# Kernel optimization log

Measured on AMD Instinct MI355X. Metric: run time of the kernel, lower is better.

The kernel has to match this reference:

```python
import jax, jax.numpy as jnp
import numpy as np

N = 100000
E = 1600000
DIN = 64
DH = 64
C = 16


def _sage_conv(x, edge_index, W_l, W_r, b):
    # PyG SAGEConv (aggr='mean'): out = lin_l(mean_{j in N(i)} x_j) + lin_r(x_i)
    src, dst = edge_index[0], edge_index[1]
    msgs = x[src]                                   # [E, D] gather
    num_nodes = x.shape[0]
    agg = jax.ops.segment_sum(msgs, dst, num_segments=num_nodes)      # [N, D]
    deg = jax.ops.segment_sum(jnp.ones((msgs.shape[0],), x.dtype), dst,
                              num_segments=num_nodes)                 # [N]
    mean = agg / jnp.maximum(deg, 1.0)[:, None]
    return mean @ W_l + b + x @ W_r


def setup_inputs() -> dict:
    key = jax.random.key(0)
    ks = jax.random.split(key, 8)
    x = jax.random.normal(ks[0], (N, DIN), dtype=jnp.float32)
    edge_index = jax.random.randint(ks[1], (2, E), 0, N, dtype=jnp.int64)
    s = 1.0 / np.sqrt(DIN)
    W1_l = jax.random.normal(ks[2], (DIN, DH), dtype=jnp.float32) * s
    W1_r = jax.random.normal(ks[3], (DIN, DH), dtype=jnp.float32) * s
    b1 = jnp.zeros((DH,), jnp.float32)
    sh = 1.0 / np.sqrt(DH)
    W2_l = jax.random.normal(ks[4], (DH, C), dtype=jnp.float32) * sh
    W2_r = jax.random.normal(ks[5], (DH, C), dtype=jnp.float32) * sh
    b2 = jnp.zeros((C,), jnp.float32)
    return {"x": x, "edge_index": edge_index, "W1_l": W1_l, "W1_r": W1_r,
            "b1": b1, "W2_l": W2_l, "W2_r": W2_r, "b2": b2}


def reference(x, edge_index, W1_l, W1_r, b1, W2_l, W2_r, b2):
    h = _sage_conv(x, edge_index, W1_l, W1_r, b1)
    h = jax.nn.relu(h)
    # dropout is identity at inference
    out = _sage_conv(h, edge_index, W2_l, W2_r, b2)
    return out
```

## Files before the change

### kernel.cpp

```cpp
#include <hip/hip_runtime.h>
#include <hip/hip_fp16.h>

#define NB 256
#define CHUNK 8192

__global__ void k_cvt(const float* __restrict__ x, __half* __restrict__ xh, int total) {
  int i = (blockIdx.x * 256 + threadIdx.x) * 8;
  if (i >= total) return;
  float4 a = *(const float4*)(x + i);
  float4 b = *(const float4*)(x + i + 4);
  __half2* dst = (__half2*)(xh + i);
  dst[0] = __floats2half2_rn(a.x, a.y);
  dst[1] = __floats2half2_rn(a.z, a.w);
  dst[2] = __floats2half2_rn(b.x, b.y);
  dst[3] = __floats2half2_rn(b.z, b.w);
}

__global__ void k_part(const int* __restrict__ srcI, const int* __restrict__ dstI,
                       int* __restrict__ gcur, int* __restrict__ pairs,
                       int E, int N, int capN, int capE) {
  __shared__ int hist[NB];
  __shared__ int base[NB];
  __shared__ int cnt[NB];
  int tid = threadIdx.x;
  int e0 = blockIdx.x * CHUNK;
  int eend = min(e0 + CHUNK, E);
  hist[tid] = 0;
  __syncthreads();
  for (int e = e0 + tid; e < eend; e += 256) {
    int d = dstI[e];
    if ((unsigned)d < (unsigned)N) atomicAdd(&hist[d / capN], 1);
  }
  __syncthreads();
  base[tid] = tid * capE + atomicAdd(&gcur[tid], hist[tid]);
  cnt[tid] = 0;
  __syncthreads();
  for (int e = e0 + tid; e < eend; e += 256) {
    int d = dstI[e];
    int s = srcI[e];
    if ((unsigned)d < (unsigned)N && (unsigned)s < (unsigned)N) {
      int b = d / capN;
      int slot = base[b] + atomicAdd(&cnt[b], 1);
      if (slot < (b + 1) * capE)
        pairs[slot] = ((d - b * capN) << 17) | s;
    }
  }
}

__launch_bounds__(512)
__global__ void k_csr(const int* __restrict__ pairs, const int* __restrict__ gcur,
                      int* __restrict__ deg, int* __restrict__ rowoff,
                      int* __restrict__ csr, int N, int capN, int capE) {
  __shared__ int hist[512];
  __shared__ int tmp[512];
  __shared__ int cur[512];
  int q = blockIdx.x;
  int tid = threadIdx.x;
  int nloc = N - q * capN;
  if (nloc > capN) nloc = capN;
  int base = q * capE;
  int cnt = gcur[q];
  if (cnt > capE) cnt = capE;
  int qbase = q * capN;
  hist[tid] = 0;
  __syncthreads();
  for (int e = tid; e < cnt; e += 512) {
    int code = pairs[base + e];
    int dl = (unsigned)code >> 17;
    if (dl < nloc) atomicAdd(&hist[dl], 1);
  }
  __syncthreads();
  int v = hist[tid];
  tmp[tid] = v;
  __syncthreads();
  for (int off = 1; off < 512; off <<= 1) {
    int t = (tid >= off) ? tmp[tid - off] : 0;
    __syncthreads();
    tmp[tid] += t;
    __syncthreads();
  }
  int ex = tmp[tid] - v;
  cur[tid] = ex;
  if (tid < nloc) {
    int i = qbase + tid;
    deg[i] = v;
    rowoff[i] = base + ex;
  }
  __syncthreads();
  for (int e = tid; e < cnt; e += 512) {
    int code = pairs[base + e];
    int dl = (unsigned)code >> 17;
    if (dl < nloc) {
      int pos = atomicAdd(&cur[dl], 1);
      csr[base + pos] = code & 0x1FFFF;
    }
  }
}

__global__ void k_agg64(const __half* __restrict__ xh, const int* __restrict__ csr,
                        const int* __restrict__ rowoff, const int* __restrict__ deg,
                        float* __restrict__ m, int n) {
  int w = (blockIdx.x * blockDim.x + threadIdx.x) >> 6;
  int lane = threadIdx.x & 63;
  if (w >= n) return;
  int start = __builtin_amdgcn_readfirstlane(rowoff[w]);
  int d = __builtin_amdgcn_readfirstlane(deg[w]);
  float a0 = 0.f, a1 = 0.f, a2 = 0.f, a3 = 0.f;
  float a4 = 0.f, a5 = 0.f, a6 = 0.f, a7 = 0.f;
  int j = 0;
  for (; j + 7 < d; j += 8) {
    int s0 = csr[start + j], s1 = csr[start + j + 1];
    int s2 = csr[start + j + 2], s3 = csr[start + j + 3];
    int s4 = csr[start + j + 4], s5 = csr[start + j + 5];
    int s6 = csr[start + j + 6], s7 = csr[start + j + 7];
    a0 += __half2float(xh[(size_t)s0 * 64 + lane]);
    a1 += __half2float(xh[(size_t)s1 * 64 + lane]);
    a2 += __half2float(xh[(size_t)s2 * 64 + lane]);
    a3 += __half2float(xh[(size_t)s3 * 64 + lane]);
    a4 += __half2float(xh[(size_t)s4 * 64 + lane]);
    a5 += __half2float(xh[(size_t)s5 * 64 + lane]);
    a6 += __half2float(xh[(size_t)s6 * 64 + lane]);
    a7 += __half2float(xh[(size_t)s7 * 64 + lane]);
  }
  for (; j + 3 < d; j += 4) {
    int s0 = csr[start + j], s1 = csr[start + j + 1];
    int s2 = csr[start + j + 2], s3 = csr[start + j + 3];
    a0 += __half2float(xh[(size_t)s0 * 64 + lane]);
    a1 += __half2float(xh[(size_t)s1 * 64 + lane]);
    a2 += __half2float(xh[(size_t)s2 * 64 + lane]);
    a3 += __half2float(xh[(size_t)s3 * 64 + lane]);
  }
  for (; j < d; ++j) a0 += __half2float(xh[(size_t)csr[start + j] * 64 + lane]);
  float inv = (d > 0) ? 1.f / (float)d : 0.f;
  m[(size_t)w * 64 + lane] = (((a0 + a1) + (a2 + a3)) + ((a4 + a5) + (a6 + a7))) * inv;
}

__launch_bounds__(256, 4)
__global__ void k_h(const float* __restrict__ m, const float* __restrict__ x,
                    const float* __restrict__ Wl, const float* __restrict__ Wr,
                    const float* __restrict__ b1, float* __restrict__ h, int n) {
  __shared__ float sAT[32 * 68];
  __shared__ float sW[32 * 64];
  int tid = threadIdx.x;
  int row0 = blockIdx.x * 64;
  int colT = tid & 15;
  int rowT = tid >> 4;
  float acc[4][4];
#pragma unroll
  for (int r = 0; r < 4; ++r)
#pragma unroll
    for (int c = 0; c < 4; ++c) acc[r][c] = 0.f;

  for (int kt = 0; kt < 4; ++kt) {
    const float* asrc = (kt < 2) ? m : x;
    const float* wsrc = (kt < 2) ? Wl : Wr;
    int ko = (kt & 1) * 32;
    __syncthreads();
    {
      int f = tid;
#pragma unroll
      for (int i = 0; i < 2; ++i, f += 256) {
        int r = f >> 3, kq = f & 7;
        int rr = row0 + r; if (rr > n - 1) rr = n - 1;
        float4 v = *(const float4*)(asrc + (size_t)rr * 64 + ko + kq * 4);
        sAT[(kq * 4 + 0) * 68 + r] = v.x;
        sAT[(kq * 4 + 1) * 68 + r] = v.y;
        sAT[(kq * 4 + 2) * 68 + r] = v.z;
        sAT[(kq * 4 + 3) * 68 + r] = v.w;
      }
      int g = tid;
#pragma unroll
      for (int i = 0; i < 2; ++i, g += 256) {
        int wr = g >> 4, cq = g & 15;
        float4 v = *(const float4*)(wsrc + (size_t)(ko + wr) * 64 + cq * 4);
        *(float4*)&sW[wr * 64 + cq * 4] = v;
      }
    }
    __syncthreads();
#pragma unroll 4
    for (int k = 0; k < 32; ++k) {
      float4 a = *(const float4*)&sAT[k * 68 + rowT * 4];
      float4 w = *(const float4*)&sW[k * 64 + colT * 4];
      acc[0][0] += a.x * w.x; acc[0][1] += a.x * w.y; acc[0][2] += a.x * w.z; acc[0][3] += a.x * w.w;
      acc[1][0] += a.y * w.x; acc[1][1] += a.y * w.y; acc[1][2] += a.y * w.z; acc[1][3] += a.y * w.w;
      acc[2][0] += a.z * w.x; acc[2][1] += a.z * w.y; acc[2][2] += a.z * w.z; acc[2][3] += a.z * w.w;
      acc[3][0] += a.w * w.x; acc[3][1] += a.w * w.y; acc[3][2] += a.w * w.z; acc[3][3] += a.w * w.w;
    }
  }
  float4 bb = *(const float4*)(b1 + colT * 4);
#pragma unroll
  for (int r = 0; r < 4; ++r) {
    int row = row0 + rowT * 4 + r;
    if (row < n) {
      float4 o;
      o.x = fmaxf(acc[r][0] + bb.x, 0.f);
      o.y = fmaxf(acc[r][1] + bb.y, 0.f);
      o.z = fmaxf(acc[r][2] + bb.z, 0.f);
      o.w = fmaxf(acc[r][3] + bb.w, 0.f);
      *(float4*)(h + (size_t)row * 64 + colT * 4) = o;
    }
  }
}

__launch_bounds__(256, 4)
__global__ void k_pq(const float* __restrict__ h, const float* __restrict__ W2l,
                     const float* __restrict__ W2r, __half* __restrict__ p16,
                     float* __restrict__ q, int n) {
  __shared__ float sAT[32 * 132];
  __shared__ float sW[32 * 32];
  int tid = threadIdx.x;
  int row0 = blockIdx.x * 128;
  int colT = tid & 7;
  int rowT = tid >> 3;
  float acc[4][4];
#pragma unroll
  for (int r = 0; r < 4; ++r)
#pragma unroll
    for (int c = 0; c < 4; ++c) acc[r][c] = 0.f;

  for (int kt = 0; kt < 2; ++kt) {
    int ko = kt * 32;
    __syncthreads();
    {
      int f = tid;
#pragma unroll
      for (int i = 0; i < 4; ++i, f += 256) {
        int r = f >> 3, kq = f & 7;
        int rr = row0 + r; if (rr > n - 1) rr = n - 1;
        float4 v = *(const float4*)(h + (size_t)rr * 64 + ko + kq * 4);
        sAT[(kq * 4 + 0) * 132 + r] = v.x;
        sAT[(kq * 4 + 1) * 132 + r] = v.y;
        sAT[(kq * 4 + 2) * 132 + r] = v.z;
        sAT[(kq * 4 + 3) * 132 + r] = v.w;
      }
      int wr = tid >> 3, cq = tid & 7;
      const float* wsrc = (cq < 4) ? W2l : W2r;
      int cc = (cq & 3) * 4;
      float4 v = *(const float4*)(wsrc + (size_t)(ko + wr) * 16 + cc);
      *(float4*)&sW[wr * 32 + cq * 4] = v;
    }
    __syncthreads();
#pragma unroll 4
    for (int k = 0; k < 32; ++k) {
      float4 a = *(const float4*)&sAT[k * 132 + rowT * 4];
      float4 w = *(const float4*)&sW[k * 32 + colT * 4];
      acc[0][0] += a.x * w.x; acc[0][1] += a.x * w.y; acc[0][2] += a.x * w.z; acc[0][3] += a.x * w.w;
      acc[1][0] += a.y * w.x; acc[1][1] += a.y * w.y; acc[1][2] += a.y * w.z; acc[1][3] += a.y * w.w;
      acc[2][0] += a.z * w.x; acc[2][1] += a.z * w.y; acc[2][2] += a.z * w.z; acc[2][3] += a.z * w.w;
      acc[3][0] += a.w * w.x; acc[3][1] += a.w * w.y; acc[3][2] += a.w * w.z; acc[3][3] += a.w * w.w;
    }
  }
#pragma unroll
  for (int r = 0; r < 4; ++r) {
    int row = row0 + rowT * 4 + r;
    if (row < n) {
      if (colT < 4) {
        __half2* dst = (__half2*)(p16 + (size_t)row * 16 + colT * 4);
        dst[0] = __floats2half2_rn(acc[r][0], acc[r][1]);
        dst[1] = __floats2half2_rn(acc[r][2], acc[r][3]);
      } else {
        *(float4*)(q + (size_t)row * 16 + (colT - 4) * 4) =
            make_float4(acc[r][0], acc[r][1], acc[r][2], acc[r][3]);
      }
    }
  }
}

__global__ void k_agg16(const __half* __restrict__ p16, const int* __restrict__ csr,
                        const int* __restrict__ rowoff, const int* __restrict__ deg,
                        const float* __restrict__ b2, float* __restrict__ out, int n) {
  int t = blockIdx.x * blockDim.x + threadIdx.x;
  int i = t >> 4;
  int dd = t & 15;
  if (i >= n) return;
  int start = rowoff[i];
  int d = deg[i];
  float a0 = 0.f, a1 = 0.f, a2 = 0.f, a3 = 0.f;
  float a4 = 0.f, a5 = 0.f, a6 = 0.f, a7 = 0.f;
  int j = 0;
  for (; j + 7 < d; j += 8) {
    int s0 = csr[start + j], s1 = csr[start + j + 1];
    int s2 = csr[start + j + 2], s3 = csr[start + j + 3];
    int s4 = csr[start + j + 4], s5 = csr[start + j + 5];
    int s6 = csr[start + j + 6], s7 = csr[start + j + 7];
    a0 += __half2float(p16[(size_t)s0 * 16 + dd]);
    a1 += __half2float(p16[(size_t)s1 * 16 + dd]);
    a2 += __half2float(p16[(size_t)s2 * 16 + dd]);
    a3 += __half2float(p16[(size_t)s3 * 16 + dd]);
    a4 += __half2float(p16[(size_t)s4 * 16 + dd]);
    a5 += __half2float(p16[(size_t)s5 * 16 + dd]);
    a6 += __half2float(p16[(size_t)s6 * 16 + dd]);
    a7 += __half2float(p16[(size_t)s7 * 16 + dd]);
  }
  for (; j + 3 < d; j += 4) {
    int s0 = csr[start + j], s1 = csr[start + j + 1];
    int s2 = csr[start + j + 2], s3 = csr[start + j + 3];
    a0 += __half2float(p16[(size_t)s0 * 16 + dd]);
    a1 += __half2float(p16[(size_t)s1 * 16 + dd]);
    a2 += __half2float(p16[(size_t)s2 * 16 + dd]);
    a3 += __half2float(p16[(size_t)s3 * 16 + dd]);
  }
  for (; j < d; ++j) a0 += __half2float(p16[(size_t)csr[start + j] * 16 + dd]);
  float inv = (d > 0) ? 1.f / (float)d : 0.f;
  out[t] = ((((a0 + a1) + (a2 + a3)) + ((a4 + a5) + (a6 + a7)))) * inv + out[t] + b2[dd];
}

extern "C" void kernel_launch(void* const* d_in, const int* in_sizes, int n_in,
                              void* d_out, int out_size, void* d_ws, size_t ws_size,
                              hipStream_t stream) {
  const float* x   = (const float*)d_in[0];
  const int*   ei  = (const int*)d_in[1];
  const float* W1l = (const float*)d_in[2];
  const float* W1r = (const float*)d_in[3];
  const float* b1  = (const float*)d_in[4];
  const float* W2l = (const float*)d_in[5];
  const float* W2r = (const float*)d_in[6];
  const float* b2  = (const float*)d_in[7];
  float* out = (float*)d_out;

  int N = in_sizes[0] / 64;
  int E = in_sizes[1] / 2;
  const int* srcI = ei;
  const int* dstI = ei + E;

  int capN = (N + NB - 1) / NB;
  int capE = E / NB + 1024;

  size_t off = 0;
  auto alloc = [&](size_t bytes) -> char* {
    char* r = (char*)d_ws + off;
    off = (off + bytes + 255) & ~(size_t)255;
    return r;
  };
  int*    deg    = (int*)alloc((size_t)N * 4);
  int*    rowoff = (int*)alloc((size_t)N * 4);
  int*    csr    = (int*)alloc((size_t)NB * capE * 4);
  int*    gcur   = (int*)alloc(NB * 4);
  __half* xh     = (__half*)alloc((size_t)N * 64 * 2);
  float*  m      = (float*)alloc((size_t)N * 64 * 4);
  float*  h      = (float*)alloc((size_t)N * 64 * 4);
  __half* p16    = (__half*)alloc((size_t)N * 16 * 2);
  int*    pairs  = (int*)h;
  if (off > ws_size) return;
  if ((size_t)NB * capE * 4 > (size_t)N * 64 * 4) return;
  if (N > (1 << 17) || capN > (1 << 9)) return;

  hipMemsetAsync(gcur, 0, NB * 4, stream);
  k_cvt<<<(N * 64 + 2047) / 2048, 256, 0, stream>>>(x, xh, N * 64);
  k_part<<<(E + CHUNK - 1) / CHUNK, 256, 0, stream>>>(srcI, dstI, gcur, pairs, E, N, capN, capE);
  k_csr<<<NB, 512, 0, stream>>>(pairs, gcur, deg, rowoff, csr, N, capN, capE);

  k_agg64<<<(N * 64 + 255) / 256, 256, 0, stream>>>(xh, csr, rowoff, deg, m, N);
  k_h<<<(N + 63) / 64, 256, 0, stream>>>(m, x, W1l, W1r, b1, h, N);

  k_pq<<<(N + 127) / 128, 256, 0, stream>>>(h, W2l, W2r, p16, out, N);
  k_agg16<<<(N * 16 + 255) / 256, 256, 0, stream>>>(p16, csr, rowoff, deg, b2, out, N);
}
```

Measured before the change: 241.3 us.

## Replace CSR build with bucketed shared-memory atomic aggregation over partitioned edge pairs

Drops the per-bucket CSR construction kernel and aggregates straight from the destination-bucketed edge pairs. Each block keeps the accumulators for its node range in LDS and adds gathered features with shared-memory float atomics. Buckets go from 256 to 512 so each block's accumulators fit in LDS, and the bucket division becomes a magic-multiply. This removes a kernel launch and the CSR write/read, at the cost of heavy LDS atomic contention, only 512 blocks in flight for the gathers, and a summation order that now depends on scheduling.

Result: slower. 855.7 us (+254.6%).

```diff
diff --git a/kernel.cpp b/kernel.cpp
--- a/kernel.cpp
+++ b/kernel.cpp
@@ -1,8 +1,9 @@
 #include <hip/hip_runtime.h>
 #include <hip/hip_fp16.h>
 
-#define NB 256
-#define CHUNK 8192
+#define NBK 512
+#define CHUNK 2048
+#define CAPN_MAX 208
 
 __global__ void k_cvt(const float* __restrict__ x, __half* __restrict__ xh, int total) {
   int i = (blockIdx.x * 256 + threadIdx.x) * 8;
@@ -16,123 +17,94 @@
   dst[3] = __floats2half2_rn(b.z, b.w);
 }
 
+__launch_bounds__(256)
 __global__ void k_part(const int* __restrict__ srcI, const int* __restrict__ dstI,
                        int* __restrict__ gcur, int* __restrict__ pairs,
-                       int E, int N, int capN, int capE) {
-  __shared__ int hist[NB];
-  __shared__ int base[NB];
-  __shared__ int cnt[NB];
+                       int E, int N, int capN, int capE, unsigned long long M) {
+  __shared__ int hist[NBK];
+  __shared__ int base[NBK];
+  __shared__ int cnt[NBK];
   int tid = threadIdx.x;
   int e0 = blockIdx.x * CHUNK;
   int eend = min(e0 + CHUNK, E);
-  hist[tid] = 0;
-  __syncthreads();
-  for (int e = e0 + tid; e < eend; e += 256) {
-    int d = dstI[e];
-    if ((unsigned)d < (unsigned)N) atomicAdd(&hist[d / capN], 1);
-  }
-  __syncthreads();
-  base[tid] = tid * capE + atomicAdd(&gcur[tid], hist[tid]);
-  cnt[tid] = 0;
-  __syncthreads();
-  for (int e = e0 + tid; e < eend; e += 256) {
-    int d = dstI[e];
-    int s = srcI[e];
-    if ((unsigned)d < (unsigned)N && (unsigned)s < (unsigned)N) {
-      int b = d / capN;
-      int slot = base[b] + atomicAdd(&cnt[b], 1);
-      if (slot < (b + 1) * capE)
-        pairs[slot] = ((d - b * capN) << 17) | s;
+  for (int i = tid; i < NBK; i += 256) hist[i] = 0;
+  __syncthreads();
+  int dc[8], bc[8];
+#pragma unroll
+  for (int j = 0; j < 8; ++j) {
+    int e = e0 + tid + j * 256;
+    int d = -1;
+    if (e < eend) {
+      int dd = dstI[e];
+      if ((unsigned)dd < (unsigned)N) d = dd;
+    }
+    int b = -1;
+    if (d >= 0) {
+      b = (int)(((unsigned long long)(unsigned)d * M) >> 34);
+      atomicAdd(&hist[b], 1);
+    }
+    dc[j] = d; bc[j] = b;
+  }
+  __syncthreads();
+  for (int i = tid; i < NBK; i += 256) {
+    base[i] = i * capE + atomicAdd(&gcur[i], hist[i]);
+    cnt[i] = 0;
+  }
+  __syncthreads();
+#pragma unroll
+  for (int j = 0; j < 8; ++j) {
+    if (dc[j] >= 0) {
+      int e = e0 + tid + j * 256;
+      int s = srcI[e];
+      if ((unsigned)s < (unsigned)N) {
+        int b = bc[j];
+        int slot = base[b] + atomicAdd(&cnt[b], 1);
+        if (slot < (b + 1) * capE)
+          pairs[slot] = ((dc[j] - b * capN) << 17) | s;
+      }
     }
   }
 }
 
 __launch_bounds__(512)
-__global__ void k_csr(const int* __restrict__ pairs, const int* __restrict__ gcur,
-                      int* __restrict__ deg, int* __restrict__ rowoff,
-                      int* __restrict__ csr, int N, int capN, int capE) {
-  __shared__ int hist[512];
-  __shared__ int tmp[512];
-  __shared__ int cur[512];
+__global__ void k_aggm(const __half* __restrict__ xh, const int* __restrict__ pairs,
+                       const int* __restrict__ gcur, float* __restrict__ m,
+                       int* __restrict__ deg, int n, int capN, int capE) {
+  __shared__ float acc[CAPN_MAX * 64];
+  __shared__ int cntL[CAPN_MAX];
   int q = blockIdx.x;
   int tid = threadIdx.x;
-  int nloc = N - q * capN;
-  if (nloc > capN) nloc = capN;
+  int qbase = q * capN;
+  int nloc = min(n - qbase, capN);
+  if (nloc <= 0) return;
   int base = q * capE;
-  int cnt = gcur[q];
-  if (cnt > capE) cnt = capE;
-  int qbase = q * capN;
-  hist[tid] = 0;
-  __syncthreads();
-  for (int e = tid; e < cnt; e += 512) {
-    int code = pairs[base + e];
-    int dl = (unsigned)code >> 17;
-    if (dl < nloc) atomicAdd(&hist[dl], 1);
-  }
-  __syncthreads();
-  int v = hist[tid];
-  tmp[tid] = v;
-  __syncthreads();
-  for (int off = 1; off < 512; off <<= 1) {
-    int t = (tid >= off) ? tmp[tid - off] : 0;
-    __syncthreads();
-    tmp[tid] += t;
-    __syncthreads();
-  }
-  int ex = tmp[tid] - v;
-  cur[tid] = ex;
-  if (tid < nloc) {
-    int i = qbase + tid;
-    deg[i] = v;
-    rowoff[i] = base + ex;
-  }
-  __syncthreads();
-  for (int e = tid; e < cnt; e += 512) {
-    int code = pairs[base + e];
-    int dl = (unsigned)code >> 17;
-    if (dl < nloc) {
-      int pos = atomicAdd(&cur[dl], 1);
-      csr[base + pos] = code & 0x1FFFF;
-    }
-  }
-}
-
-__global__ void k_agg64(const __half* __restrict__ xh, const int* __restrict__ csr,
-                        const int* __restrict__ rowoff, const int* __restrict__ deg,
-                        float* __restrict__ m, int n) {
-  int w = (blockIdx.x * blockDim.x + threadIdx.x) >> 6;
-  int lane = threadIdx.x & 63;
-  if (w >= n) return;
-  int start = __builtin_amdgcn_readfirstlane(rowoff[w]);
-  int d = __builtin_amdgcn_readfirstlane(deg[w]);
-  float a0 = 0.f, a1 = 0.f, a2 = 0.f, a3 = 0.f;
-  float a4 = 0.f, a5 = 0.f, a6 = 0.f, a7 = 0.f;
-  int j = 0;
-  for (; j + 7 < d; j += 8) {
-    int s0 = csr[start + j], s1 = csr[start + j + 1];
-    int s2 = csr[start + j + 2], s3 = csr[start + j + 3];
-    int s4 = csr[start + j + 4], s5 = csr[start + j + 5];
-    int s6 = csr[start + j + 6], s7 = csr[start + j + 7];
-    a0 += __half2float(xh[(size_t)s0 * 64 + lane]);
-    a1 += __half2float(xh[(size_t)s1 * 64 + lane]);
-    a2 += __half2float(xh[(size_t)s2 * 64 + lane]);
-    a3 += __half2float(xh[(size_t)s3 * 64 + lane]);
-    a4 += __half2float(xh[(size_t)s4 * 64 + lane]);
-    a5 += __half2float(xh[(size_t)s5 * 64 + lane]);
-    a6 += __half2float(xh[(size_t)s6 * 64 + lane]);
-    a7 += __half2float(xh[(size_t)s7 * 64 + lane]);
-  }
-  for (; j + 3 < d; j += 4) {
-    int s0 = csr[start + j], s1 = csr[start + j + 1];
-    int s2 = csr[start + j + 2], s3 = csr[start + j + 3];
-    a0 += __half2float(xh[(size_t)s0 * 64 + lane]);
-    a1 += __half2float(xh[(size_t)s1 * 64 + lane]);
-    a2 += __half2float(xh[(size_t)s2 * 64 + lane]);
-    a3 += __half2float(xh[(size_t)s3 * 64 + lane]);
-  }
-  for (; j < d; ++j) a0 += __half2float(xh[(size_t)csr[start + j] * 64 + lane]);
-  float inv = (d > 0) ? 1.f / (float)d : 0.f;
-  m[(size_t)w * 64 + lane] = (((a0 + a1) + (a2 + a3)) + ((a4 + a5) + (a6 + a7))) * inv;
+  int ecnt = min(gcur[q], capE);
+  for (int i = tid; i < nloc * 64; i += 512) acc[i] = 0.f;
+  for (int i = tid; i < nloc; i += 512) cntL[i] = 0;
+  __syncthreads();
+  int wid = tid >> 6, lane = tid & 63;
+  for (int e0 = wid * 8; e0 < ecnt; e0 += 64) {
+#pragma unroll
+    for (int j = 0; j < 8; ++j) {
+      int e = e0 + j;
+      if (e < ecnt) {
+        int code = pairs[base + e];
+        int dl = (unsigned)code >> 17;
+        int s = code & 0x1FFFF;
+        float v = __half2float(xh[(size_t)s * 64 + lane]);
+        atomicAdd(&acc[dl * 64 + lane], v);
+        if (lane == 0) atomicAdd(&cntL[dl], 1);
+      }
+    }
+  }
+  __syncthreads();
+  for (int i = tid; i < nloc * 64; i += 512) {
+    int r = i >> 6;
+    int c = cntL[r];
+    float inv = (c > 0) ? 1.f / (float)c : 0.f;
+    m[(size_t)(qbase + r) * 64 + (i & 63)] = acc[i] * inv;
+  }
+  for (int i = tid; i < nloc; i += 512) deg[qbase + i] = cntL[i];
 }
 
 __launch_bounds__(256, 4)
@@ -266,43 +238,44 @@
   }
 }
 
-__global__ void k_agg16(const __half* __restrict__ p16, const int* __restrict__ csr,
-                        const int* __restrict__ rowoff, const int* __restrict__ deg,
-                        const float* __restrict__ b2, float* __restrict__ out, int n) {
-  int t = blockIdx.x * blockDim.x + threadIdx.x;
-  int i = t >> 4;
-  int dd = t & 15;
-  if (i >= n) return;
-  int start = rowoff[i];
-  int d = deg[i];
-  float a0 = 0.f, a1 = 0.f, a2 = 0.f, a3 = 0.f;
-  float a4 = 0.f, a5 = 0.f, a6 = 0.f, a7 = 0.f;
-  int j = 0;
-  for (; j + 7 < d; j += 8) {
-    int s0 = csr[start + j], s1 = csr[start + j + 1];
-    int s2 = csr[start + j + 2], s3 = csr[start + j + 3];
-    int s4 = csr[start + j + 4], s5 = csr[start + j + 5];
-    int s6 = csr[start + j + 6], s7 = csr[start + j + 7];
-    a0 += __half2float(p16[(size_t)s0 * 16 + dd]);
-    a1 += __half2float(p16[(size_t)s1 * 16 + dd]);
-    a2 += __half2float(p16[(size_t)s2 * 16 + dd]);
-    a3 += __half2float(p16[(size_t)s3 * 16 + dd]);
-    a4 += __half2float(p16[(size_t)s4 * 16 + dd]);
-    a5 += __half2float(p16[(size_t)s5 * 16 + dd]);
-    a6 += __half2float(p16[(size_t)s6 * 16 + dd]);
-    a7 += __half2float(p16[(size_t)s7 * 16 + dd]);
-  }
-  for (; j + 3 < d; j += 4) {
-    int s0 = csr[start + j], s1 = csr[start + j + 1];
-    int s2 = csr[start + j + 2], s3 = csr[start + j + 3];
-    a0 += __half2float(p16[(size_t)s0 * 16 + dd]);
-    a1 += __half2float(p16[(size_t)s1 * 16 + dd]);
-    a2 += __half2float(p16[(size_t)s2 * 16 + dd]);
-    a3 += __half2float(p16[(size_t)s3 * 16 + dd]);
-  }
-  for (; j < d; ++j) a0 += __half2float(p16[(size_t)csr[start + j] * 16 + dd]);
-  float inv = (d > 0) ? 1.f / (float)d : 0.f;
-  out[t] = ((((a0 + a1) + (a2 + a3)) + ((a4 + a5) + (a6 + a7)))) * inv + out[t] + b2[dd];
+__launch_bounds__(256)
+__global__ void k_aggq(const __half* __restrict__ p16, const int* __restrict__ pairs,
+                       const int* __restrict__ gcur, const int* __restrict__ deg,
+                       const float* __restrict__ b2, float* __restrict__ out,
+                       int n, int capN, int capE) {
+  __shared__ float acc[CAPN_MAX * 16];
+  int q = blockIdx.x;
+  int tid = threadIdx.x;
+  int qbase = q * capN;
+  int nloc = min(n - qbase, capN);
+  if (nloc <= 0) return;
+  int base = q * capE;
+  int ecnt = min(gcur[q], capE);
+  for (int i = tid; i < nloc * 16; i += 256) acc[i] = 0.f;
+  __syncthreads();
+  int wid = tid >> 6, lane = tid & 63;
+  int esub = lane >> 4, dim = lane & 15;
+  for (int e0 = wid * 16; e0 < ecnt; e0 += 64) {
+#pragma unroll
+    for (int j = 0; j < 4; ++j) {
+      int e = e0 + j * 4 + esub;
+      if (e < ecnt) {
+        int code = pairs[base + e];
+        int dl = (unsigned)code >> 17;
+        int s = code & 0x1FFFF;
+        float v = __half2float(p16[(size_t)s * 16 + dim]);
+        atomicAdd(&acc[dl * 16 + dim], v);
+      }
+    }
+  }
+  __syncthreads();
+  for (int i = tid; i < nloc * 16; i += 256) {
+    int r = i >> 4, dd = i & 15;
+    int dg = deg[qbase + r];
+    float inv = (dg > 0) ? 1.f / (float)dg : 0.f;
+    size_t o = (size_t)(qbase + r) * 16 + dd;
+    out[o] = acc[i] * inv + out[o] + b2[dd];
+  }
 }
 
 extern "C" void kernel_launch(void* const* d_in, const int* in_sizes, int n_in,
@@ -323,8 +296,9 @@
   const int* srcI = ei;
   const int* dstI = ei + E;
 
-  int capN = (N + NB - 1) / NB;
-  int capE = E / NB + 1024;
+  int capN = (N + NBK - 1) / NBK;
+  int capE = E / NBK + 512;
+  unsigned long long M = ((1ULL << 34) + capN - 1) / (unsigned long long)capN;
 
   size_t off = 0;
   auto alloc = [&](size_t bytes) -> char* {
@@ -332,27 +306,23 @@
     off = (off + bytes + 255) & ~(size_t)255;
     return r;
   };
-  int*    deg    = (int*)alloc((size_t)N * 4);
-  int*    rowoff = (int*)alloc((size_t)N * 4);
-  int*    csr    = (int*)alloc((size_t)NB * capE * 4);
-  int*    gcur   = (int*)alloc(NB * 4);
-  __half* xh     = (__half*)alloc((size_t)N * 64 * 2);
-  float*  m      = (float*)alloc((size_t)N * 64 * 4);
-  float*  h      = (float*)alloc((size_t)N * 64 * 4);
-  __half* p16    = (__half*)alloc((size_t)N * 16 * 2);
-  int*    pairs  = (int*)h;
+  int*    deg   = (int*)alloc((size_t)N * 4);
+  int*    gcur  = (int*)alloc(NBK * 4);
+  int*    pairs = (int*)alloc((size_t)NBK * capE * 4);
+  __half* xh    = (__half*)alloc((size_t)N * 64 * 2);
+  float*  m     = (float*)alloc((size_t)N * 64 * 4);
+  float*  h     = (float*)alloc((size_t)N * 64 * 4);
+  __half* p16   = (__half*)alloc((size_t)N * 16 * 2);
   if (off > ws_size) return;
-  if ((size_t)NB * capE * 4 > (size_t)N * 64 * 4) return;
-  if (N > (1 << 17) || capN > (1 << 9)) return;
-
-  hipMemsetAsync(gcur, 0, NB * 4, stream);
+  if (N > (1 << 17) || capN > CAPN_MAX) return;
+
+  hipMemsetAsync(gcur, 0, NBK * 4, stream);
   k_cvt<<<(N * 64 + 2047) / 2048, 256, 0, stream>>>(x, xh, N * 64);
-  k_part<<<(E + CHUNK - 1) / CHUNK, 256, 0, stream>>>(srcI, dstI, gcur, pairs, E, N, capN, capE);
-  k_csr<<<NB, 512, 0, stream>>>(pairs, gcur, deg, rowoff, csr, N, capN, capE);
-
-  k_agg64<<<(N * 64 + 255) / 256, 256, 0, stream>>>(xh, csr, rowoff, deg, m, N);
+  k_part<<<(E + CHUNK - 1) / CHUNK, 256, 0, stream>>>(srcI, dstI, gcur, pairs, E, N, capN, capE, M);
+
+  k_aggm<<<NBK, 512, 0, stream>>>(xh, pairs, gcur, m, deg, N, capN, capE);
   k_h<<<(N + 63) / 64, 256, 0, stream>>>(m, x, W1l, W1r, b1, h, N);
 
   k_pq<<<(N + 127) / 128, 256, 0, stream>>>(h, W2l, W2r, p16, out, N);
-  k_agg16<<<(N * 16 + 255) / 256, 256, 0, stream>>>(p16, csr, rowoff, deg, b2, out, N);
-}
+  k_aggq<<<NBK, 256, 0, stream>>>(p16, pairs, gcur, deg, b2, out, N, capN, capE);
+}
```

## Vectorize gathers in aggregation kernels and register-cache partition edges

Applied to the files above, without the earlier changes.

The 64-wide aggregation now has each lane load 4 halves (8 bytes) from one of 4 edges processed in parallel, then reduces across lane groups with shuffles. The 16-wide aggregation is remapped from 16 threads per node to a full wavefront per node, using the same vectorized gather and shuffle reduction. k_part uses smaller chunks, keeps dst and bucket values in registers so dstI is not read twice, and gets explicit launch bounds. These changes aim to raise memory-level parallelism on the random gathers and to cut redundant index loads, at the cost of shuffle reductions and idle lanes on low-degree nodes.

After: 261.5 us. +8.4%, slower.

```diff
diff --git a/kernel.cpp b/kernel.cpp
--- a/kernel.cpp
+++ b/kernel.cpp
@@ -2,7 +2,7 @@
 #include <hip/hip_fp16.h>
 
 #define NB 256
-#define CHUNK 8192
+#define CHUNK 2048
 
 __global__ void k_cvt(const float* __restrict__ x, __half* __restrict__ xh, int total) {
   int i = (blockIdx.x * 256 + threadIdx.x) * 8;
@@ -16,6 +16,7 @@
   dst[3] = __floats2half2_rn(b.z, b.w);
 }
 
+__launch_bounds__(256)
 __global__ void k_part(const int* __restrict__ srcI, const int* __restrict__ dstI,
                        int* __restrict__ gcur, int* __restrict__ pairs,
                        int E, int N, int capN, int capE) {
@@ -27,22 +28,37 @@
   int eend = min(e0 + CHUNK, E);
   hist[tid] = 0;
   __syncthreads();
-  for (int e = e0 + tid; e < eend; e += 256) {
-    int d = dstI[e];
-    if ((unsigned)d < (unsigned)N) atomicAdd(&hist[d / capN], 1);
+  int dc[8], bc[8];
+#pragma unroll
+  for (int j = 0; j < 8; ++j) {
+    int e = e0 + tid + j * 256;
+    int d = -1;
+    if (e < eend) {
+      int dd = dstI[e];
+      if ((unsigned)dd < (unsigned)N) d = dd;
+    }
+    int b = -1;
+    if (d >= 0) {
+      b = d / capN;
+      atomicAdd(&hist[b], 1);
+    }
+    dc[j] = d; bc[j] = b;
   }
   __syncthreads();
   base[tid] = tid * capE + atomicAdd(&gcur[tid], hist[tid]);
   cnt[tid] = 0;
   __syncthreads();
-  for (int e = e0 + tid; e < eend; e += 256) {
-    int d = dstI[e];
-    int s = srcI[e];
-    if ((unsigned)d < (unsigned)N && (unsigned)s < (unsigned)N) {
-      int b = d / capN;
-      int slot = base[b] + atomicAdd(&cnt[b], 1);
-      if (slot < (b + 1) * capE)
-        pairs[slot] = ((d - b * capN) << 17) | s;
+#pragma unroll
+  for (int j = 0; j < 8; ++j) {
+    if (dc[j] >= 0) {
+      int e = e0 + tid + j * 256;
+      int s = srcI[e];
+      if ((unsigned)s < (unsigned)N) {
+        int b = bc[j];
+        int slot = base[b] + atomicAdd(&cnt[b], 1);
+        if (slot < (b + 1) * capE)
+          pairs[slot] = ((dc[j] - b * capN) << 17) | s;
+      }
     }
   }
 }
@@ -105,34 +121,33 @@
   if (w >= n) return;
   int start = __builtin_amdgcn_readfirstlane(rowoff[w]);
   int d = __builtin_amdgcn_readfirstlane(deg[w]);
+  int g = lane >> 4, c = lane & 15;
+  int end = start + d;
   float a0 = 0.f, a1 = 0.f, a2 = 0.f, a3 = 0.f;
-  float a4 = 0.f, a5 = 0.f, a6 = 0.f, a7 = 0.f;
-  int j = 0;
-  for (; j + 7 < d; j += 8) {
-    int s0 = csr[start + j], s1 = csr[start + j + 1];
-    int s2 = csr[start + j + 2], s3 = csr[start + j + 3];
-    int s4 = csr[start + j + 4], s5 = csr[start + j + 5];
-    int s6 = csr[start + j + 6], s7 = csr[start + j + 7];
-    a0 += __half2float(xh[(size_t)s0 * 64 + lane]);
-    a1 += __half2float(xh[(size_t)s1 * 64 + lane]);
-    a2 += __half2float(xh[(size_t)s2 * 64 + lane]);
-    a3 += __half2float(xh[(size_t)s3 * 64 + lane]);
-    a4 += __half2float(xh[(size_t)s4 * 64 + lane]);
-    a5 += __half2float(xh[(size_t)s5 * 64 + lane]);
-    a6 += __half2float(xh[(size_t)s6 * 64 + lane]);
-    a7 += __half2float(xh[(size_t)s7 * 64 + lane]);
-  }
-  for (; j + 3 < d; j += 4) {
-    int s0 = csr[start + j], s1 = csr[start + j + 1];
-    int s2 = csr[start + j + 2], s3 = csr[start + j + 3];
-    a0 += __half2float(xh[(size_t)s0 * 64 + lane]);
-    a1 += __half2float(xh[(size_t)s1 * 64 + lane]);
-    a2 += __half2float(xh[(size_t)s2 * 64 + lane]);
-    a3 += __half2float(xh[(size_t)s3 * 64 + lane]);
-  }
-  for (; j < d; ++j) a0 += __half2float(xh[(size_t)csr[start + j] * 64 + lane]);
-  float inv = (d > 0) ? 1.f / (float)d : 0.f;
-  m[(size_t)w * 64 + lane] = (((a0 + a1) + (a2 + a3)) + ((a4 + a5) + (a6 + a7))) * inv;
+  for (int eb = start; eb < end; eb += 32) {
+#pragma unroll
+    for (int j = 0; j < 8; ++j) {
+      int e = eb + j * 4 + g;
+      if (e < end) {
+        int s = csr[e];
+        uint2 u = *(const uint2*)(xh + (size_t)s * 64 + c * 4);
+        __half2 h0 = *(__half2*)&u.x;
+        __half2 h1 = *(__half2*)&u.y;
+        float2 f0 = __half22float2(h0);
+        float2 f1 = __half22float2(h1);
+        a0 += f0.x; a1 += f0.y; a2 += f1.x; a3 += f1.y;
+      }
+    }
+  }
+  a0 += __shfl_xor(a0, 16); a1 += __shfl_xor(a1, 16);
+  a2 += __shfl_xor(a2, 16); a3 += __shfl_xor(a3, 16);
+  a0 += __shfl_xor(a0, 32); a1 += __shfl_xor(a1, 32);
+  a2 += __shfl_xor(a2, 32); a3 += __shfl_xor(a3, 32);
+  if (lane < 16) {
+    float inv = (d > 0) ? 1.f / (float)d : 0.f;
+    *(float4*)(m + (size_t)w * 64 + c * 4) =
+        make_float4(a0 * inv, a1 * inv, a2 * inv, a3 * inv);
+  }
 }
 
 __launch_bounds__(256, 4)
@@ -269,40 +284,47 @@
 __global__ void k_agg16(const __half* __restrict__ p16, const int* __restrict__ csr,
                         const int* __restrict__ rowoff, const int* __restrict__ deg,
                         const float* __restrict__ b2, float* __restrict__ out, int n) {
-  int t = blockIdx.x * blockDim.x + threadIdx.x;
-  int i = t >> 4;
-  int dd = t & 15;
+  int i = (blockIdx.x * blockDim.x + threadIdx.x) >> 6;
+  int lane = threadIdx.x & 63;
   if (i >= n) return;
-  int start = rowoff[i];
-  int d = deg[i];
+  int start = __builtin_amdgcn_readfirstlane(rowoff[i]);
+  int d = __builtin_amdgcn_readfirstlane(deg[i]);
+  int g = lane >> 2, c = lane & 3;
+  int end = start + d;
   float a0 = 0.f, a1 = 0.f, a2 = 0.f, a3 = 0.f;
-  float a4 = 0.f, a5 = 0.f, a6 = 0.f, a7 = 0.f;
-  int j = 0;
-  for (; j + 7 < d; j += 8) {
-    int s0 = csr[start + j], s1 = csr[start + j + 1];
-    int s2 = csr[start + j + 2], s3 = csr[start + j + 3];
-    int s4 = csr[start + j + 4], s5 = csr[start + j + 5];
-    int s6 = csr[start + j + 6], s7 = csr[start + j + 7];
-    a0 += __half2float(p16[(size_t)s0 * 16 + dd]);
-    a1 += __half2float(p16[(size_t)s1 * 16 + dd]);
-    a2 += __half2float(p16[(size_t)s2 * 16 + dd]);
-    a3 += __half2float(p16[(size_t)s3 * 16 + dd]);
-    a4 += __half2float(p16[(size_t)s4 * 16 + dd]);
-    a5 += __half2float(p16[(size_t)s5 * 16 + dd]);
-    a6 += __half2float(p16[(size_t)s6 * 16 + dd]);
-    a7 += __half2float(p16[(size_t)s7 * 16 + dd]);
-  }
-  for (; j + 3 < d; j += 4) {
-    int s0 = csr[start + j], s1 = csr[start + j + 1];
-    int s2 = csr[start + j + 2], s3 = csr[start + j + 3];
-    a0 += __half2float(p16[(size_t)s0 * 16 + dd]);
-    a1 += __half2float(p16[(size_t)s1 * 16 + dd]);
-    a2 += __half2float(p16[(size_t)s2 * 16 + dd]);
-    a3 += __half2float(p16[(size_t)s3 * 16 + dd]);
-  }
-  for (; j < d; ++j) a0 += __half2float(p16[(size_t)csr[start + j] * 16 + dd]);
-  float inv = (d > 0) ? 1.f / (float)d : 0.f;
-  out[t] = ((((a0 + a1) + (a2 + a3)) + ((a4 + a5) + (a6 + a7)))) * inv + out[t] + b2[dd];
+  for (int eb = start; eb < end; eb += 32) {
+#pragma unroll
+    for (int j = 0; j < 2; ++j) {
+      int e = eb + j * 16 + g;
+      if (e < end) {
+        int s = csr[e];
+        uint2 u = *(const uint2*)(p16 + (size_t)s * 16 + c * 4);
+        __half2 h0 = *(__half2*)&u.x;
+        __half2 h1 = *(__half2*)&u.y;
+        float2 f0 = __half22float2(h0);
+        float2 f1 = __half22float2(h1);
+        a0 += f0.x; a1 += f0.y; a2 += f1.x; a3 += f1.y;
+      }
+    }
+  }
+  a0 += __shfl_xor(a0, 4);  a1 += __shfl_xor(a1, 4);
+  a2 += __shfl_xor(a2, 4);  a3 += __shfl_xor(a3, 4);
+  a0 += __shfl_xor(a0, 8);  a1 += __shfl_xor(a1, 8);
+  a2 += __shfl_xor(a2, 8);  a3 += __shfl_xor(a3, 8);
+  a0 += __shfl_xor(a0, 16); a1 += __shfl_xor(a1, 16);
+  a2 += __shfl_xor(a2, 16); a3 += __shfl_xor(a3, 16);
+  a0 += __shfl_xor(a0, 32); a1 += __shfl_xor(a1, 32);
+  a2 += __shfl_xor(a2, 32); a3 += __shfl_xor(a3, 32);
+  if (lane < 4) {
+    float inv = (d > 0) ? 1.f / (float)d : 0.f;
+    size_t o = (size_t)i * 16 + c * 4;
+    float4 qv = *(const float4*)(out + o);
+    float4 bb = *(const float4*)(b2 + c * 4);
+    *(float4*)(out + o) = make_float4(a0 * inv + qv.x + bb.x,
+                                      a1 * inv + qv.y + bb.y,
+                                      a2 * inv + qv.z + bb.z,
+                                      a3 * inv + qv.w + bb.w);
+  }
 }
 
 extern "C" void kernel_launch(void* const* d_in, const int* in_sizes, int n_in,
@@ -354,5 +376,5 @@
   k_h<<<(N + 63) / 64, 256, 0, stream>>>(m, x, W1l, W1r, b1, h, N);
 
   k_pq<<<(N + 127) / 128, 256, 0, stream>>>(h, W2l, W2r, p16, out, N);
-  k_agg16<<<(N * 16 + 255) / 256, 256, 0, stream>>>(p16, csr, rowoff, deg, b2, out, N);
-}
+  k_agg16<<<(N * 64 + 255) / 256, 256, 0, stream>>>(p16, csr, rowoff, deg, b2, out, N);
+}
```

## Fuse layer-1 and layer-2 linear kernels and merge fp16 convert into partitioning

Applied to the files above, without the earlier changes.

Merges k_h and k_pq into a single kernel that keeps the ReLU'd hidden tile in shared memory and multiplies it by the layer-2 weights directly, so the N x 64 fp32 h array is never written to or read back from global memory. Also folds the fp16 conversion of x into the edge-partition kernel as a grid-stride loop. The partition kernel now uses smaller chunks with dst values and bucket ids cached in registers, so dstI is read only once. The cost is more launched blocks with more atomics on gcur, higher shared-memory use in the fused GEMM kernel, and the pairs buffer now aliasing m.

Result: faster. 227.0 us (-5.9%).

```diff
diff --git a/kernel.cpp b/kernel.cpp
--- a/kernel.cpp
+++ b/kernel.cpp
@@ -2,47 +2,65 @@
 #include <hip/hip_fp16.h>
 
 #define NB 256
-#define CHUNK 8192
-
-__global__ void k_cvt(const float* __restrict__ x, __half* __restrict__ xh, int total) {
-  int i = (blockIdx.x * 256 + threadIdx.x) * 8;
-  if (i >= total) return;
-  float4 a = *(const float4*)(x + i);
-  float4 b = *(const float4*)(x + i + 4);
-  __half2* dst = (__half2*)(xh + i);
-  dst[0] = __floats2half2_rn(a.x, a.y);
-  dst[1] = __floats2half2_rn(a.z, a.w);
-  dst[2] = __floats2half2_rn(b.x, b.y);
-  dst[3] = __floats2half2_rn(b.z, b.w);
-}
-
-__global__ void k_part(const int* __restrict__ srcI, const int* __restrict__ dstI,
-                       int* __restrict__ gcur, int* __restrict__ pairs,
-                       int E, int N, int capN, int capE) {
+#define CHUNK 2048
+
+__launch_bounds__(256)
+__global__ void k_partcvt(const int* __restrict__ srcI, const int* __restrict__ dstI,
+                          const float* __restrict__ x, __half* __restrict__ xh, int total,
+                          int* __restrict__ gcur, int* __restrict__ pairs,
+                          int E, int N, int capN, int capE) {
   __shared__ int hist[NB];
   __shared__ int base[NB];
   __shared__ int cnt[NB];
   int tid = threadIdx.x;
+
+  int gsz = gridDim.x * 256;
+  for (int i = blockIdx.x * 256 + tid; i * 8 < total; i += gsz) {
+    int i8 = i * 8;
+    float4 a = *(const float4*)(x + i8);
+    float4 b = *(const float4*)(x + i8 + 4);
+    __half2* dst = (__half2*)(xh + i8);
+    dst[0] = __floats2half2_rn(a.x, a.y);
+    dst[1] = __floats2half2_rn(a.z, a.w);
+    dst[2] = __floats2half2_rn(b.x, b.y);
+    dst[3] = __floats2half2_rn(b.z, b.w);
+  }
+
   int e0 = blockIdx.x * CHUNK;
   int eend = min(e0 + CHUNK, E);
   hist[tid] = 0;
   __syncthreads();
-  for (int e = e0 + tid; e < eend; e += 256) {
-    int d = dstI[e];
-    if ((unsigned)d < (unsigned)N) atomicAdd(&hist[d / capN], 1);
+  int dc[8], bc[8];
+#pragma unroll
+  for (int j = 0; j < 8; ++j) {
+    int e = e0 + tid + j * 256;
+    int d = -1;
+    if (e < eend) {
+      int dd = dstI[e];
+      if ((unsigned)dd < (unsigned)N) d = dd;
+    }
+    int b = -1;
+    if (d >= 0) {
+      b = d / capN;
+      atomicAdd(&hist[b], 1);
+    }
+    dc[j] = d; bc[j] = b;
   }
   __syncthreads();
   base[tid] = tid * capE + atomicAdd(&gcur[tid], hist[tid]);
   cnt[tid] = 0;
   __syncthreads();
-  for (int e = e0 + tid; e < eend; e += 256) {
-    int d = dstI[e];
-    int s = srcI[e];
-    if ((unsigned)d < (unsigned)N && (unsigned)s < (unsigned)N) {
-      int b = d / capN;
-      int slot = base[b] + atomicAdd(&cnt[b], 1);
-      if (slot < (b + 1) * capE)
-        pairs[slot] = ((d - b * capN) << 17) | s;
+#pragma unroll
+  for (int j = 0; j < 8; ++j) {
+    if (dc[j] >= 0) {
+      int e = e0 + tid + j * 256;
+      int s = srcI[e];
+      if ((unsigned)s < (unsigned)N) {
+        int b = bc[j];
+        int slot = base[b] + atomicAdd(&cnt[b], 1);
+        if (slot < (b + 1) * capE)
+          pairs[slot] = ((dc[j] - b * capN) << 17) | s;
+      }
     }
   }
 }
@@ -136,15 +154,33 @@
 }
 
 __launch_bounds__(256, 4)
-__global__ void k_h(const float* __restrict__ m, const float* __restrict__ x,
-                    const float* __restrict__ Wl, const float* __restrict__ Wr,
-                    const float* __restrict__ b1, float* __restrict__ h, int n) {
-  __shared__ float sAT[32 * 68];
-  __shared__ float sW[32 * 64];
+__global__ void k_hpq(const float* __restrict__ m, const float* __restrict__ x,
+                      const float* __restrict__ W1l, const float* __restrict__ W1r,
+                      const float* __restrict__ b1, const float* __restrict__ W2l,
+                      const float* __restrict__ W2r, __half* __restrict__ p16,
+                      float* __restrict__ q, int n) {
+  __shared__ float smem[6400];
+  float* sAT = smem;
+  float* sW  = smem + 2176;
+  float* hT  = smem;
+  float* sW2 = smem + 4352;
   int tid = threadIdx.x;
   int row0 = blockIdx.x * 64;
   int colT = tid & 15;
   int rowT = tid >> 4;
+
+  {
+    int g = tid;
+#pragma unroll
+    for (int i = 0; i < 2; ++i, g += 256) {
+      int wr = g >> 3, cq = g & 7;
+      const float* wsrc = (cq < 4) ? W2l : W2r;
+      int cc = (cq & 3) * 4;
+      float4 v = *(const float4*)(wsrc + (size_t)wr * 16 + cc);
+      *(float4*)&sW2[wr * 32 + cq * 4] = v;
+    }
+  }
+
   float acc[4][4];
 #pragma unroll
   for (int r = 0; r < 4; ++r)
@@ -153,7 +189,7 @@
 
   for (int kt = 0; kt < 4; ++kt) {
     const float* asrc = (kt < 2) ? m : x;
-    const float* wsrc = (kt < 2) ? Wl : Wr;
+    const float* wsrc = (kt < 2) ? W1l : W1r;
     int ko = (kt & 1) * 32;
     __syncthreads();
     {
@@ -187,80 +223,48 @@
       acc[3][0] += a.w * w.x; acc[3][1] += a.w * w.y; acc[3][2] += a.w * w.z; acc[3][3] += a.w * w.w;
     }
   }
-  float4 bb = *(const float4*)(b1 + colT * 4);
-#pragma unroll
-  for (int r = 0; r < 4; ++r) {
-    int row = row0 + rowT * 4 + r;
+  __syncthreads();
+
+  {
+    float4 bb = *(const float4*)(b1 + colT * 4);
+    float bbv[4] = {bb.x, bb.y, bb.z, bb.w};
+#pragma unroll
+    for (int c = 0; c < 4; ++c) {
+      float4 hv;
+      hv.x = fmaxf(acc[0][c] + bbv[c], 0.f);
+      hv.y = fmaxf(acc[1][c] + bbv[c], 0.f);
+      hv.z = fmaxf(acc[2][c] + bbv[c], 0.f);
+      hv.w = fmaxf(acc[3][c] + bbv[c], 0.f);
+      *(float4*)&hT[(colT * 4 + c) * 68 + rowT * 4] = hv;
+    }
+  }
+  __syncthreads();
+
+  int colT2 = tid & 7;
+  int rowT2 = tid >> 3;
+  float acc2[2][4];
+#pragma unroll
+  for (int r = 0; r < 2; ++r)
+#pragma unroll
+    for (int c = 0; c < 4; ++c) acc2[r][c] = 0.f;
+#pragma unroll 4
+  for (int k = 0; k < 64; ++k) {
+    float2 a = *(const float2*)&hT[k * 68 + rowT2 * 2];
+    float4 w = *(const float4*)&sW2[k * 32 + colT2 * 4];
+    acc2[0][0] += a.x * w.x; acc2[0][1] += a.x * w.y; acc2[0][2] += a.x * w.z; acc2[0][3] += a.x * w.w;
+    acc2[1][0] += a.y * w.x; acc2[1][1] += a.y * w.y; acc2[1][2] += a.y * w.z; acc2[1][3] += a.y * w.w;
+  }
+#pragma unroll
+  for (int r = 0; r < 2; ++r) {
+    int row = row0 + rowT2 * 2 + r;
     if (row < n) {
-      float4 o;
-      o.x = fmaxf(acc[r][0] + bb.x, 0.f);
-      o.y = fmaxf(acc[r][1] + bb.y, 0.f);
-      o.z = fmaxf(acc[r][2] + bb.z, 0.f);
-      o.w = fmaxf(acc[r][3] + bb.w, 0.f);
-      *(float4*)(h + (size_t)row * 64 + colT * 4) = o;
-    }
-  }
-}
-
-__launch_bounds__(256, 4)
-__global__ void k_pq(const float* __restrict__ h, const float* __restrict__ W2l,
-                     const float* __restrict__ W2r, __half* __restrict__ p16,
-                     float* __restrict__ q, int n) {
-  __shared__ float sAT[32 * 132];
-  __shared__ float sW[32 * 32];
-  int tid = threadIdx.x;
-  int row0 = blockIdx.x * 128;
-  int colT = tid & 7;
-  int rowT = tid >> 3;
-  float acc[4][4];
-#pragma unroll
-  for (int r = 0; r < 4; ++r)
-#pragma unroll
-    for (int c = 0; c < 4; ++c) acc[r][c] = 0.f;
-
-  for (int kt = 0; kt < 2; ++kt) {
-    int ko = kt * 32;
-    __syncthreads();
-    {
-      int f = tid;
-#pragma unroll
-      for (int i = 0; i < 4; ++i, f += 256) {
-        int r = f >> 3, kq = f & 7;
-        int rr = row0 + r; if (rr > n - 1) rr = n - 1;
-        float4 v = *(const float4*)(h + (size_t)rr * 64 + ko + kq * 4);
-        sAT[(kq * 4 + 0) * 132 + r] = v.x;
-        sAT[(kq * 4 + 1) * 132 + r] = v.y;
-        sAT[(kq * 4 + 2) * 132 + r] = v.z;
-        sAT[(kq * 4 + 3) * 132 + r] = v.w;
-      }
-      int wr = tid >> 3, cq = tid & 7;
-      const float* wsrc = (cq < 4) ? W2l : W2r;
-      int cc = (cq & 3) * 4;
-      float4 v = *(const float4*)(wsrc + (size_t)(ko + wr) * 16 + cc);
-      *(float4*)&sW[wr * 32 + cq * 4] = v;
-    }
-    __syncthreads();
-#pragma unroll 4
-    for (int k = 0; k < 32; ++k) {
-      float4 a = *(const float4*)&sAT[k * 132 + rowT * 4];
-      float4 w = *(const float4*)&sW[k * 32 + colT * 4];
-      acc[0][0] += a.x * w.x; acc[0][1] += a.x * w.y; acc[0][2] += a.x * w.z; acc[0][3] += a.x * w.w;
-      acc[1][0] += a.y * w.x; acc[1][1] += a.y * w.y; acc[1][2] += a.y * w.z; acc[1][3] += a.y * w.w;
-      acc[2][0] += a.z * w.x; acc[2][1] += a.z * w.y; acc[2][2] += a.z * w.z; acc[2][3] += a.z * w.w;
-      acc[3][0] += a.w * w.x; acc[3][1] += a.w * w.y; acc[3][2] += a.w * w.z; acc[3][3] += a.w * w.w;
-    }
-  }
-#pragma unroll
-  for (int r = 0; r < 4; ++r) {
-    int row = row0 + rowT * 4 + r;
-    if (row < n) {
-      if (colT < 4) {
-        __half2* dst = (__half2*)(p16 + (size_t)row * 16 + colT * 4);
-        dst[0] = __floats2half2_rn(acc[r][0], acc[r][1]);
-        dst[1] = __floats2half2_rn(acc[r][2], acc[r][3]);
+      if (colT2 < 4) {
+        __half2* dst = (__half2*)(p16 + (size_t)row * 16 + colT2 * 4);
+        dst[0] = __floats2half2_rn(acc2[r][0], acc2[r][1]);
+        dst[1] = __floats2half2_rn(acc2[r][2], acc2[r][3]);
       } else {
-        *(float4*)(q + (size_t)row * 16 + (colT - 4) * 4) =
-            make_float4(acc[r][0], acc[r][1], acc[r][2], acc[r][3]);
+        *(float4*)(q + (size_t)row * 16 + (colT2 - 4) * 4) =
+            make_float4(acc2[r][0], acc2[r][1], acc2[r][2], acc2[r][3]);
       }
     }
   }
@@ -338,21 +342,19 @@
   int*    gcur   = (int*)alloc(NB * 4);
   __half* xh     = (__half*)alloc((size_t)N * 64 * 2);
   float*  m      = (float*)alloc((size_t)N * 64 * 4);
-  float*  h      = (float*)alloc((size_t)N * 64 * 4);
   __half* p16    = (__half*)alloc((size_t)N * 16 * 2);
-  int*    pairs  = (int*)h;
+  int*    pairs  = (int*)m;
   if (off > ws_size) return;
   if ((size_t)NB * capE * 4 > (size_t)N * 64 * 4) return;
   if (N > (1 << 17) || capN > (1 << 9)) return;
 
   hipMemsetAsync(gcur, 0, NB * 4, stream);
-  k_cvt<<<(N * 64 + 2047) / 2048, 256, 0, stream>>>(x, xh, N * 64);
-  k_part<<<(E + CHUNK - 1) / CHUNK, 256, 0, stream>>>(srcI, dstI, gcur, pairs, E, N, capN, capE);
+  k_partcvt<<<(E + CHUNK - 1) / CHUNK, 256, 0, stream>>>(srcI, dstI, x, xh, N * 64,
+                                                         gcur, pairs, E, N, capN, capE);
   k_csr<<<NB, 512, 0, stream>>>(pairs, gcur, deg, rowoff, csr, N, capN, capE);
 
   k_agg64<<<(N * 64 + 255) / 256, 256, 0, stream>>>(xh, csr, rowoff, deg, m, N);
-  k_h<<<(N + 63) / 64, 256, 0, stream>>>(m, x, W1l, W1r, b1, h, N);
-
-  k_pq<<<(N + 127) / 128, 256, 0, stream>>>(h, W2l, W2r, p16, out, N);
+  k_hpq<<<(N + 63) / 64, 256, 0, stream>>>(m, x, W1l, W1r, b1, W2l, W2r, p16, out, N);
+
   k_agg16<<<(N * 16 + 255) / 256, 256, 0, stream>>>(p16, csr, rowoff, deg, b2, out, N);
 }
```
